# Kernel tuning notes

Measured on AMD Instinct MI355X. Metric: run time of the kernel, lower is better.

The kernel has to match this reference:

```python
import jax, jax.numpy as jnp
import numpy as np

DEPTH = 8
DIM = 1024
DI = 2 * DIM        # d_inner (expand=2)
DSTATE = 16         # d_state
DCONV = 4           # conv kernel width
DTRANK = DIM // 16  # dt_rank = ceil(d_model/16) = 64
B = 2
L = 2048
EPS = 1e-5


def setup_inputs() -> dict:
    key = jax.random.key(0)
    ks = jax.random.split(key, 8)
    s = 0.02
    A_log = jnp.broadcast_to(
        jnp.log(jnp.arange(1, DSTATE + 1, dtype=jnp.float32)), (DEPTH, DI, DSTATE)
    )
    return {
        "x": jax.random.normal(ks[0], (B, L, DIM), jnp.float32),
        "in_proj_w": jax.random.normal(ks[1], (DEPTH, 2 * DI, DIM), jnp.float32) * s,
        "conv_w": jax.random.normal(ks[2], (DEPTH, DI, DCONV), jnp.float32) * s,
        "conv_b": jnp.zeros((DEPTH, DI), jnp.float32),
        "x_proj_w": jax.random.normal(ks[3], (DEPTH, DTRANK + 2 * DSTATE, DI), jnp.float32) * s,
        "dt_proj_w": jax.random.normal(ks[4], (DEPTH, DI, DTRANK), jnp.float32) * s,
        "dt_proj_b": jax.random.normal(ks[5], (DEPTH, DI), jnp.float32) * 0.1,
        "A_log": A_log + 0.0,
        "D": jnp.ones((DEPTH, DI), jnp.float32),
        "out_proj_w": jax.random.normal(ks[6], (DEPTH, DIM, DI), jnp.float32) * s,
        "rms_w": jnp.ones((DEPTH, DIM), jnp.float32),
    }


def _selective_scan(xs, delta, Bm, Cm, A):
    # xs, delta: [B, L, DI]; Bm, Cm: [B, L, DSTATE]; A: [DI, DSTATE]
    def step(h, t):
        dt, Bt, Ct, xt = t  # [B,DI], [B,N], [B,N], [B,DI]
        dA = jnp.exp(dt[:, :, None] * A)                      # [B,DI,N]
        h = dA * h + (dt * xt)[:, :, None] * Bt[:, None, :]   # [B,DI,N]
        y = jnp.einsum('bdn,bn->bd', h, Ct)                   # [B,DI]
        return h, y

    h0 = jnp.zeros((xs.shape[0], xs.shape[2], A.shape[1]), xs.dtype)
    ts = (delta.transpose(1, 0, 2), Bm.transpose(1, 0, 2),
          Cm.transpose(1, 0, 2), xs.transpose(1, 0, 2))
    _, ys = jax.lax.scan(step, h0, ts)  # ys: [L,B,DI]
    return ys.transpose(1, 0, 2)


def _mamba(x, Wi, cw, cb, Wx, Wdt, bdt, A_log, Dp, Wo):
    # in_proj (no bias): [B,L,DIM] -> [B,L,2*DI]
    xz = jnp.einsum('bld,ed->ble', x, Wi)
    xs, z = jnp.split(xz, 2, axis=-1)
    # depthwise causal conv1d, kernel DCONV, left pad DCONV-1
    xc = jax.lax.conv_general_dilated(
        xs.transpose(0, 2, 1), cw[:, None, :], (1,), [(DCONV - 1, 0)],
        dimension_numbers=('NCH', 'OIH', 'NCH'), feature_group_count=DI)
    xs = jax.nn.silu(xc + cb[None, :, None]).transpose(0, 2, 1)  # [B,L,DI]
    # x_proj -> dt, B, C
    xdbl = jnp.einsum('bld,ed->ble', xs, Wx)
    dt, Bm, Cm = jnp.split(xdbl, [DTRANK, DTRANK + DSTATE], axis=-1)
    delta = jax.nn.softplus(jnp.einsum('blr,dr->bld', dt, Wdt) + bdt)  # [B,L,DI]
    A = -jnp.exp(A_log)  # [DI, DSTATE]
    y = _selective_scan(xs, delta, Bm, Cm, A) + xs * Dp
    y = y * jax.nn.silu(z)
    return jnp.einsum('bld,ed->ble', y, Wo)  # out_proj, no bias


def _rmsnorm(x, w):
    return x * jax.lax.rsqrt(jnp.mean(x * x, axis=-1, keepdims=True) + EPS) * w


def reference(x, in_proj_w, conv_w, conv_b, x_proj_w, dt_proj_w, dt_proj_b,
              A_log, D, out_proj_w, rms_w):
    for i in range(DEPTH):
        x = _mamba(x, in_proj_w[i], conv_w[i], conv_b[i], x_proj_w[i],
                   dt_proj_w[i], dt_proj_b[i], A_log[i], D[i], out_proj_w[i])
        x = _rmsnorm(x, rms_w[i])
    return x
```

## Files before the change

kernel.cpp:

```cpp
#include <hip/hip_runtime.h>
#include <cstddef>

#define DEPTH  8
#define DIMM   1024
#define DI     2048
#define NST    16
#define DCONVK 4
#define DTRANK 64
#define BB     2
#define LL     2048
#define MM     (BB*LL)
#define BD     (BB*DI)
#define CHK    32
#define LC     (LL/CHK)
#define LOG2E  1.44269504088896f

typedef __attribute__((ext_vector_type(8))) short bf16x8;
typedef __attribute__((ext_vector_type(4))) float f32x4;

__device__ __forceinline__ unsigned short f2bf(float f) {
  unsigned int u = __float_as_uint(f);
  unsigned int r = (u + 0x7fffu + ((u >> 16) & 1u)) >> 16;
  return (unsigned short)r;
}
__device__ __forceinline__ float bf2f(unsigned short h) {
  return __uint_as_float(((unsigned int)h) << 16);
}

__global__ __launch_bounds__(256) void cvt2_k(const float* __restrict__ x,
                                              unsigned short* __restrict__ p,
                                              size_t n) {
  size_t i = ((size_t)blockIdx.x * 256 + threadIdx.x) * 4;
  float4 v = *(const float4*)(x + i);
  float vv[4] = {v.x, v.y, v.z, v.w};
  unsigned short u1[4], u2[4];
#pragma unroll
  for (int k = 0; k < 4; ++k) {
    unsigned short h1 = f2bf(vv[k]);
    u1[k] = h1;
    u2[k] = f2bf(vv[k] - bf2f(h1));
  }
  *(ushort4*)(p + i)     = make_ushort4(u1[0], u1[1], u1[2], u1[3]);
  *(ushort4*)(p + n + i) = make_ushort4(u2[0], u2[1], u2[2], u2[3]);
}

template <int BN, int NSPLIT>
__global__ __launch_bounds__(512, 2) void gemm3ph(
    const unsigned short* __restrict__ Ap, int lda_a, int pstr_a,
    const unsigned short* __restrict__ Bp, int lda_b, int pstr_b,
    float* __restrict__ C0, float* __restrict__ C1, int N, int Ktot) {
  constexpr int BM  = 256;
  constexpr int BF  = BN / 64;
  constexpr int BL  = BN / 128;
  constexpr int RA1 = BM * 32;
  constexpr int RB0 = 2 * BM * 32;
  constexpr int RB1 = RB0 + BN * 32;
  constexpr int BUFS = (2 * BM + 2 * BN) * 32;
  __shared__ unsigned short S[2 * BUFS];

  const int t  = threadIdx.x;
  const int w  = t >> 6;
  const int l  = t & 63;
  const int lm = l & 15;
  const int qs = ((l >> 4) << 3) ^ (((lm >> 1) & 3) << 3);

  const int nx   = gridDim.x;
  const int nwg  = nx * gridDim.y;
  const int flat = blockIdx.y * nx + blockIdx.x;
  const int swz  = (flat & 7) * (nwg >> 3) + (flat >> 3);
  const int m0 = (swz / nx) * BM;
  const int n0 = (swz % nx) * BN;
  const int z  = (NSPLIT == 2) ? blockIdx.z : 0;
  const int KS = Ktot / NSPLIT;

  const int wm = (w & 1) << 7;
  const int wn = (w >> 1) * (BN / 4);

  const int rr = t >> 2;
  const int kq = ((t & 3) ^ ((rr >> 1) & 3)) << 3;
  const unsigned short* srcA = Ap + (size_t)(m0 + rr) * lda_a + (size_t)z * KS + kq;
  const unsigned short* srcB = Bp + (size_t)(n0 + rr) * lda_b + (size_t)z * KS + kq;
  const size_t a128 = (size_t)128 * lda_a;
  const size_t b128 = (size_t)128 * lda_b;
  const int dbase = (w << 6) * 8;

#define GI(p_, off_)                                                           \
  __builtin_amdgcn_global_load_lds(                                            \
      (const __attribute__((address_space(1))) unsigned int*)(p_),             \
      (__attribute__((address_space(3))) unsigned int*)&S[bnext + (off_) + dbase], \
      16, 0, 0)

#define GI_PH0(kb_)                                                            \
  { GI(srcA + (kb_), 0); GI(srcA + a128 + (kb_), 4096);                        \
    GI(srcB + (kb_), RB0);                                                     \
    if constexpr (BL == 2) GI(srcB + b128 + (kb_), RB0 + 4096); }

#define GI_PH1(kb_)                                                            \
  { GI(srcB + (size_t)pstr_b + (kb_), RB1);                                    \
    if constexpr (BL == 2) GI(srcB + (size_t)pstr_b + b128 + (kb_), RB1 + 4096); }

#define GI_PH2(kb_)                                                            \
  { GI(srcA + (size_t)pstr_a + (kb_), RA1);                                    \
    GI(srcA + (size_t)pstr_a + a128 + (kb_), RA1 + 4096); }

  f32x4 acc[8][BF];
#pragma unroll
  for (int i = 0; i < 8; ++i)
#pragma unroll
    for (int j = 0; j < BF; ++j) acc[i][j] = (f32x4){0.f, 0.f, 0.f, 0.f};

  {
    const int bnext = 0;
    GI_PH0((size_t)0);
    GI_PH1((size_t)0);
    GI_PH2((size_t)0);
  }
  if constexpr (BN == 256) asm volatile("s_waitcnt vmcnt(4)" ::: "memory");
  else                     asm volatile("s_waitcnt vmcnt(3)" ::: "memory");
  __builtin_amdgcn_s_barrier();

  const int NT = KS >> 5;
#pragma unroll 2
  for (int ti = 0; ti < NT; ++ti) {
    const int bcur  = (ti & 1) ? BUFS : 0;
    const int bnext = (ti & 1) ? 0 : BUFS;
    const size_t kb = (size_t)((ti + 1 < NT) ? (ti + 1) : 0) * 32;
    const unsigned short* Sb = &S[bcur];
    bf16x8 a[8], b0[BF], b1[BF];

#pragma unroll
    for (int i = 0; i < 8; ++i)
      a[i] = *(const bf16x8*)&Sb[(wm + i * 16 + lm) * 32 + qs];
#pragma unroll
    for (int j = 0; j < BF; ++j)
      b0[j] = *(const bf16x8*)&Sb[RB0 + (wn + j * 16 + lm) * 32 + qs];
    GI_PH0(kb);
    if constexpr (BN == 256) asm volatile("s_waitcnt vmcnt(6)" ::: "memory");
    else                     asm volatile("s_waitcnt vmcnt(5)" ::: "memory");
    __builtin_amdgcn_s_barrier();
    asm volatile("s_waitcnt lgkmcnt(0)" ::: "memory");
    __builtin_amdgcn_s_setprio(1);
#pragma unroll
    for (int i = 0; i < 8; ++i)
#pragma unroll
      for (int j = 0; j < BF; ++j)
        acc[i][j] = __builtin_amdgcn_mfma_f32_16x16x32_bf16(a[i], b0[j], acc[i][j], 0, 0, 0);
    __builtin_amdgcn_s_setprio(0);
    __builtin_amdgcn_s_barrier();

#pragma unroll
    for (int j = 0; j < BF; ++j)
      b1[j] = *(const bf16x8*)&Sb[RB1 + (wn + j * 16 + lm) * 32 + qs];
    GI_PH1(kb);
    if constexpr (BN == 256) asm volatile("s_waitcnt vmcnt(6)" ::: "memory");
    else                     asm volatile("s_waitcnt vmcnt(4)" ::: "memory");
    __builtin_amdgcn_s_barrier();
    asm volatile("s_waitcnt lgkmcnt(0)" ::: "memory");
    __builtin_amdgcn_s_setprio(1);
#pragma unroll
    for (int i = 0; i < 8; ++i)
#pragma unroll
      for (int j = 0; j < BF; ++j)
        acc[i][j] = __builtin_amdgcn_mfma_f32_16x16x32_bf16(a[i], b1[j], acc[i][j], 0, 0, 0);
    __builtin_amdgcn_s_setprio(0);
    __builtin_amdgcn_s_barrier();

#pragma unroll
    for (int i = 0; i < 8; ++i)
      a[i] = *(const bf16x8*)&Sb[RA1 + (wm + i * 16 + lm) * 32 + qs];
    GI_PH2(kb);
    if constexpr (BN == 256) asm volatile("s_waitcnt vmcnt(4)" ::: "memory");
    else                     asm volatile("s_waitcnt vmcnt(3)" ::: "memory");
    __builtin_amdgcn_s_barrier();
    asm volatile("s_waitcnt lgkmcnt(0)" ::: "memory");
    __builtin_amdgcn_s_setprio(1);
#pragma unroll
    for (int i = 0; i < 8; ++i)
#pragma unroll
      for (int j = 0; j < BF; ++j)
        acc[i][j] = __builtin_amdgcn_mfma_f32_16x16x32_bf16(a[i], b0[j], acc[i][j], 0, 0, 0);
    __builtin_amdgcn_s_setprio(0);
    __builtin_amdgcn_s_barrier();
  }
#undef GI_PH2
#undef GI_PH1
#undef GI_PH0
#undef GI

  float* Cc = (NSPLIT == 2 && blockIdx.z) ? C1 : C0;
  const int row0 = (l >> 4) << 2;
#pragma unroll
  for (int i = 0; i < 8; ++i)
#pragma unroll
    for (int j = 0; j < BF; ++j)
#pragma unroll
      for (int r = 0; r < 4; ++r) {
        int m = m0 + wm + i * 16 + row0 + r;
        int n = n0 + wn + j * 16 + lm;
        Cc[(size_t)m * N + n] = acc[i][j][r];
      }
}

__global__ __launch_bounds__(256) void dtproj_mp(const unsigned short* __restrict__ Ap,
                                                 const unsigned short* __restrict__ Bp,
                                                 const float* __restrict__ bdt,
                                                 float* __restrict__ Cd) {
  __shared__ unsigned short S[32768];
  const int t  = threadIdx.x;
  const int w  = t >> 6;
  const int l  = t & 63;
  const int lm = l & 15;
  const int q8 = (l >> 4) << 3;
  const int qs = q8 ^ (((lm >> 1) & 3) << 3);
  const int m0 = blockIdx.y * 128;
  const int n0 = blockIdx.x * 128;
  const int wm = (w & 1) << 6;
  const int wn = (w >> 1) << 6;

#pragma unroll
  for (int it = 0; it < 16; ++it) {
    int c  = it * 256 + t;
    int kt = c >> 11;
    int c2 = c & 2047;
    const unsigned short* base;
    int r, aslot;
    if (c2 < 1024) {
      int p = c2 >> 9; int wi = c2 & 511; r = wi >> 2; aslot = wi & 3;
      base = Ap + (size_t)p * (MM * 64) + (size_t)(m0 + r) * 64;
    } else {
      int c3 = c2 - 1024;
      int p = c3 >> 9; int wi = c3 & 511; r = wi >> 2; aslot = wi & 3;
      base = Bp + (size_t)p * (DI * 64) + (size_t)(n0 + r) * 64;
    }
    int kq = (aslot ^ ((r >> 1) & 3)) << 3;
    __builtin_amdgcn_global_load_lds(
        (const __attribute__((address_space(1))) unsigned int*)(base + kt * 32 + kq),
        (__attribute__((address_space(3))) unsigned int*)&S[(size_t)(it * 256 + (w << 6)) * 8],
        16, 0, 0);
  }
  __syncthreads();

  f32x4 acc[4][4];
#pragma unroll
  for (int i = 0; i < 4; ++i)
#pragma unroll
    for (int j = 0; j < 4; ++j) acc[i][j] = (f32x4){0.f, 0.f, 0.f, 0.f};

#pragma unroll
  for (int kt = 0; kt < 2; ++kt) {
    const int RA = kt * 16384;
    const int RB = kt * 16384 + 8192;
    bf16x8 a0[4], aX[4], b0[4];
#pragma unroll
    for (int i = 0; i < 4; ++i)
      a0[i] = *(const bf16x8*)&S[RA + (wm + i * 16 + lm) * 32 + qs];
#pragma unroll
    for (int j = 0; j < 4; ++j)
      b0[j] = *(const bf16x8*)&S[RB + (wn + j * 16 + lm) * 32 + qs];
#pragma unroll
    for (int i = 0; i < 4; ++i)
#pragma unroll
      for (int j = 0; j < 4; ++j)
        acc[i][j] = __builtin_amdgcn_mfma_f32_16x16x32_bf16(a0[i], b0[j], acc[i][j], 0, 0, 0);
#pragma unroll
    for (int j = 0; j < 4; ++j)
      aX[j] = *(const bf16x8*)&S[RB + 4096 + (wn + j * 16 + lm) * 32 + qs];
#pragma unroll
    for (int i = 0; i < 4; ++i)
#pragma unroll
      for (int j = 0; j < 4; ++j)
        acc[i][j] = __builtin_amdgcn_mfma_f32_16x16x32_bf16(a0[i], aX[j], acc[i][j], 0, 0, 0);
#pragma unroll
    for (int i = 0; i < 4; ++i)
      aX[i] = *(const bf16x8*)&S[RA + 4096 + (wm + i * 16 + lm) * 32 + qs];
#pragma unroll
    for (int i = 0; i < 4; ++i)
#pragma unroll
      for (int j = 0; j < 4; ++j)
        acc[i][j] = __builtin_amdgcn_mfma_f32_16x16x32_bf16(aX[i], b0[j], acc[i][j], 0, 0, 0);
  }

  const int row0 = (l >> 4) << 2;
#pragma unroll
  for (int j = 0; j < 4; ++j) {
    int n = n0 + wn + j * 16 + lm;
    float bv = bdt[n];
#pragma unroll
    for (int i = 0; i < 4; ++i)
#pragma unroll
      for (int r = 0; r < 4; ++r) {
        int m = m0 + wm + i * 16 + row0 + r;
        float x = acc[i][j][r] + bv;
        Cd[(size_t)m * DI + n] = fmaxf(x, 0.f) + log1pf(expf(-fabsf(x)));
      }
  }
}

#define XPN 96
__global__ __launch_bounds__(256) void xproj_part_k(const float* __restrict__ A,
                                                    const float* __restrict__ W,
                                                    float* __restrict__ Cp) {
  __shared__ float As[16][128];
  __shared__ float Ws[16][XPN];
  const int t  = threadIdx.x;
  const int tx = t & 15;
  const int ty = t >> 4;
  const int m0 = blockIdx.x * 128;
  const int kb = blockIdx.y * 256;
  float acc[8][6];
#pragma unroll
  for (int i = 0; i < 8; ++i)
#pragma unroll
    for (int j = 0; j < 6; ++j) acc[i][j] = 0.f;

  for (int k0 = kb; k0 < kb + 256; k0 += 16) {
#pragma unroll
    for (int e = t; e < 512; e += 256) {
      int r = e >> 2, cq = (e & 3) << 2;
      float4 v = *(const float4*)(A + (size_t)(m0 + r) * DI + k0 + cq);
      As[cq+0][r] = v.x; As[cq+1][r] = v.y; As[cq+2][r] = v.z; As[cq+3][r] = v.w;
    }
    for (int e = t; e < 384; e += 256) {
      int r = e >> 2, cq = (e & 3) << 2;
      float4 v = *(const float4*)(W + (size_t)r * DI + k0 + cq);
      Ws[cq+0][r] = v.x; Ws[cq+1][r] = v.y; Ws[cq+2][r] = v.z; Ws[cq+3][r] = v.w;
    }
    __syncthreads();
#pragma unroll
    for (int kk = 0; kk < 16; ++kk) {
      float a[8], b[6];
#pragma unroll
      for (int i = 0; i < 8; ++i) a[i] = As[kk][ty*8 + i];
#pragma unroll
      for (int j = 0; j < 6; ++j) b[j] = Ws[kk][tx*6 + j];
#pragma unroll
      for (int i = 0; i < 8; ++i)
#pragma unroll
        for (int j = 0; j < 6; ++j) acc[i][j] += a[i] * b[j];
    }
    __syncthreads();
  }
  float* cp = Cp + (size_t)blockIdx.y * MM * XPN;
#pragma unroll
  for (int i = 0; i < 8; ++i)
#pragma unroll
    for (int j = 0; j < 6; ++j)
      cp[(size_t)(m0 + ty*8 + i) * XPN + tx*6 + j] = acc[i][j];
}

__global__ __launch_bounds__(256) void xproj_red_k(const float* __restrict__ Cp,
                                                   float* __restrict__ o,
                                                   unsigned short* __restrict__ dtp) {
  int i = blockIdx.x * 256 + threadIdx.x;
  float s = 0.f;
#pragma unroll
  for (int ks = 0; ks < 8; ++ks) s += Cp[(size_t)ks * (MM * XPN) + i];
  o[i] = s;
  int m = i / 96, col = i - m * 96;
  if (col < DTRANK) {
    unsigned short h1 = f2bf(s);
    dtp[(size_t)m * DTRANK + col] = h1;
    dtp[(size_t)MM * DTRANK + (size_t)m * DTRANK + col] = f2bf(s - bf2f(h1));
  }
}

__device__ __forceinline__ float fast_silu(float x) {
  return x * __builtin_amdgcn_rcpf(1.f + exp2f(-LOG2E * x));
}

__global__ __launch_bounds__(256) void conv_silu_k(const float* __restrict__ xz,
                                                   const float* __restrict__ cw,
                                                   const float* __restrict__ cb,
                                                   float* __restrict__ xc) {
  int idx = blockIdx.x * 256 + threadIdx.x;
  int c  = idx & (DI - 1);
  int bl = idx >> 11;
  int l  = bl & (LL - 1);
  float acc = cb[c];
#pragma unroll
  for (int k = 0; k < DCONVK; ++k) {
    int ls = l - (DCONVK - 1) + k;
    if (ls >= 0)
      acc += xz[(size_t)(bl - (DCONVK - 1) + k) * (2*DI) + c] * cw[c*DCONVK + k];
  }
  xc[idx] = fast_silu(acc);
}

__global__ __launch_bounds__(256) void scan_pass1(const float* __restrict__ delta,
                                                  const float* __restrict__ xc,
                                                  const float* __restrict__ xdbl,
                                                  const float* __restrict__ A_log,
                                                  float* __restrict__ Hc,
                                                  float* __restrict__ Sdt) {
  const int t  = threadIdx.x;
  const int c  = blockIdx.x >> 6;
  const int g  = blockIdx.x & 63;
  const int q  = t >> 2;
  const int nq = t & 3;
  const int ch = g * 64 + q;
  const int b  = ch >> 11;
  const int d  = ch & (DI - 1);
  const size_t rowbase = (size_t)b * LL + (size_t)c * LC;

  __shared__ float Bs[LC * 16];
  { int row = t >> 2, seg = t & 3;
    *(float4*)&Bs[row * 16 + seg * 4] =
        *(const float4*)(xdbl + (rowbase + row) * 96 + DTRANK + seg * 4);
  }
  __syncthreads();

  float4 al = *(const float4*)(A_log + (size_t)d * NST + nq * 4);
  const float Av0 = -expf(al.x) * LOG2E, Av1 = -expf(al.y) * LOG2E;
  const float Av2_ = -expf(al.z) * LOG2E, Av3 = -expf(al.w) * LOG2E;
  float h0 = 0.f, h1 = 0.f, h2 = 0.f, h3 = 0.f, S = 0.f;

#define P1_SU 4
  float aD[P1_SU], aX[P1_SU];
  float bD[P1_SU], bX[P1_SU];

#define P1_LOAD(l0, D_, X_)                                            \
  { _Pragma("unroll")                                                  \
    for (int u = 0; u < P1_SU; ++u) {                                  \
      size_t bl = rowbase + (l0) + u;                                  \
      D_[u] = delta[bl * DI + d];                                      \
      X_[u] = xc[bl * DI + d];                                         \
    } }

#define P1_COMP(l0, D_, X_)                                            \
  { _Pragma("unroll")                                                  \
    for (int u = 0; u < P1_SU; ++u) {                                  \
      float4 Bv = *(const float4*)&Bs[((l0) + u) * 16 + nq * 4];       \
      float dt = D_[u], uB = dt * X_[u];                               \
      h0 = fmaf(exp2f(dt * Av0), h0, uB * Bv.x);                       \
      h1 = fmaf(exp2f(dt * Av1), h1, uB * Bv.y);                       \
      h2 = fmaf(exp2f(dt * Av2_), h2, uB * Bv.z);                      \
      h3 = fmaf(exp2f(dt * Av3), h3, uB * Bv.w);                       \
      S += dt;                                                         \
    } }

  P1_LOAD(0, aD, aX);
  for (int l0 = 0; l0 < LC; l0 += 2 * P1_SU) {
    P1_LOAD(l0 + P1_SU, bD, bX);
    P1_COMP(l0, aD, aX);
    if (l0 + 2 * P1_SU < LC) P1_LOAD(l0 + 2 * P1_SU, aD, aX);
    P1_COMP(l0 + P1_SU, bD, bX);
  }
#undef P1_LOAD
#undef P1_COMP
  size_t hi = ((size_t)c * BD + ch) * NST + nq * 4;
  float4 hv; hv.x = h0; hv.y = h1; hv.z = h2; hv.w = h3;
  *(float4*)(Hc + hi) = hv;
  if (nq == 0) Sdt[(size_t)c * BD + ch] = S;
}

__global__ __launch_bounds__(256) void scan_pass2(float* __restrict__ Hc,
                                                  const float* __restrict__ Sdt,
                                                  const float* __restrict__ A_log) {
  const int g  = blockIdx.x * 256 + threadIdx.x;
  const int n  = g & (NST - 1);
  const int ch = g >> 4;
  const int d  = ch & (DI - 1);
  const float Av2 = -expf(A_log[d * NST + n]) * LOG2E;
  float Sv[CHK];
#pragma unroll
  for (int c = 0; c < CHK; ++c) Sv[c] = Sdt[(size_t)c * BD + ch];
  float h = 0.f;
  float tmp = Hc[(size_t)ch * NST + n];
#pragma unroll
  for (int c = 0; c < CHK; ++c) {
    size_t idx = ((size_t)c * BD + ch) * NST + n;
    float tnext = (c + 1 < CHK) ? Hc[((size_t)(c+1) * BD + ch) * NST + n] : 0.f;
    Hc[idx] = h;
    h = fmaf(exp2f(Av2 * Sv[c]), h, tmp);
    tmp = tnext;
  }
}

__global__ __launch_bounds__(256) void scan_pass3(const float* __restrict__ delta,
                                                  const float* __restrict__ xc,
                                                  const float* __restrict__ xdbl,
                                                  const float* __restrict__ A_log,
                                                  float* __restrict__ xzp,
                                                  const float* __restrict__ Dp,
                                                  const float* __restrict__ Hc) {
  const int t  = threadIdx.x;
  const int c  = blockIdx.x >> 6;
  const int g  = blockIdx.x & 63;
  const int q  = t >> 2;
  const int nq = t & 3;
  const int ch = g * 64 + q;
  const int b  = ch >> 11;
  const int d  = ch & (DI - 1);
  const int dbs = (g & 31) * 64;
  const size_t rowbase = (size_t)b * LL + (size_t)c * LC;

  __shared__ float BCs[LC * 32];
  __shared__ unsigned short Y1s[LC][64];
  __shared__ unsigned short Y2s[LC][64];
  {
#pragma unroll
    for (int e = t; e < 512; e += 256) {
      int row = e >> 3, seg = e & 7;
      *(float4*)&BCs[row * 32 + seg * 4] =
          *(const float4*)(xdbl + (rowbase + row) * 96 + DTRANK + seg * 4);
    }
  }
  __syncthreads();

  float4 al = *(const float4*)(A_log + (size_t)d * NST + nq * 4);
  const float Av0 = -expf(al.x) * LOG2E, Av1 = -expf(al.y) * LOG2E;
  const float Av2_ = -expf(al.z) * LOG2E, Av3 = -expf(al.w) * LOG2E;
  const float Dv = Dp[d];
  float4 hv = *(const float4*)(Hc + ((size_t)c * BD + ch) * NST + nq * 4);
  float h0 = hv.x, h1 = hv.y, h2 = hv.z, h3 = hv.w;

#define P3_SU 2
  float aD[P3_SU], aX[P3_SU], aZ[P3_SU];
  float bD[P3_SU], bX[P3_SU], bZ[P3_SU];

#define P3_LOAD(l0, D_, X_, Z_)                                        \
  { _Pragma("unroll")                                                  \
    for (int u = 0; u < P3_SU; ++u) {                                  \
      size_t bl = rowbase + (l0) + u;                                  \
      D_[u] = delta[bl * DI + d];                                      \
      X_[u] = xc[bl * DI + d];                                         \
      Z_[u] = xzp[bl * (2*DI) + DI + d];                               \
    } }

#define P3_COMP(l0, D_, X_, Z_)                                        \
  { _Pragma("unroll")                                                  \
    for (int u = 0; u < P3_SU; ++u) {                                  \
      float4 Bv = *(const float4*)&BCs[((l0) + u) * 32 + nq * 4];      \
      float4 Cv = *(const float4*)&BCs[((l0) + u) * 32 + 16 + nq * 4]; \
      float dt = D_[u], uB = dt * X_[u];                               \
      h0 = fmaf(exp2f(dt * Av0), h0, uB * Bv.x);                       \
      h1 = fmaf(exp2f(dt * Av1), h1, uB * Bv.y);                       \
      h2 = fmaf(exp2f(dt * Av2_), h2, uB * Bv.z);                      \
      h3 = fmaf(exp2f(dt * Av3), h3, uB * Bv.w);                       \
      float s = fmaf(h1, Cv.y, h0 * Cv.x);                             \
      float t2 = fmaf(h3, Cv.w, h2 * Cv.z);                            \
      s += t2;                                                         \
      s += __shfl_xor(s, 1, 4);                                        \
      s += __shfl_xor(s, 2, 4);                                        \
      if (nq == 0) {                                                   \
        float yv = (s + X_[u] * Dv) * fast_silu(Z_[u]);                \
        unsigned short y1 = f2bf(yv);                                  \
        Y1s[(l0) + u][q] = y1;                                         \
        Y2s[(l0) + u][q] = f2bf(yv - bf2f(y1));                        \
      }                                                                \
    } }

  P3_LOAD(0, aD, aX, aZ);
  for (int l0 = 0; l0 < LC; l0 += 2 * P3_SU) {
    P3_LOAD(l0 + P3_SU, bD, bX, bZ);
    P3_COMP(l0, aD, aX, aZ);
    if (l0 + 2 * P3_SU < LC) P3_LOAD(l0 + 2 * P3_SU, aD, aX, aZ);
    P3_COMP(l0 + P3_SU, bD, bX, bZ);
  }
#undef P3_LOAD
#undef P3_COMP
  __syncthreads();

  unsigned short* yp = (unsigned short*)xzp;
#pragma unroll
  for (int e = t; e < LC * 16; e += 256) {
    int row = e >> 4, seg = (e & 15) << 2;
    size_t base = (rowbase + row) * 8192 + dbs + seg;
    *(ushort4*)(yp + base)        = *(const ushort4*)&Y1s[row][seg];
    *(ushort4*)(yp + base + 2048) = *(const ushort4*)&Y2s[row][seg];
  }
}

template <bool PLANES>
__global__ __launch_bounds__(256) void rmsnorm_k(const float* __restrict__ x,
                                                 const float* __restrict__ x2,
                                                 const float* __restrict__ w,
                                                 float* __restrict__ o,
                                                 unsigned short* __restrict__ op) {
  int row = blockIdx.x;
  const float* xr  = x  + (size_t)row * DIMM;
  const float* x2r = x2 + (size_t)row * DIMM;
  float s = 0.f;
  for (int i = threadIdx.x; i < DIMM; i += 256) {
    float v = xr[i] + x2r[i]; s += v * v;
  }
#pragma unroll
  for (int off = 32; off > 0; off >>= 1) s += __shfl_xor(s, off, 64);
  __shared__ float red[4];
  if ((threadIdx.x & 63) == 0) red[threadIdx.x >> 6] = s;
  __syncthreads();
  float tot = red[0] + red[1] + red[2] + red[3];
  float scale = rsqrtf(tot * (1.0f / DIMM) + 1e-5f);
  for (int i = threadIdx.x; i < DIMM; i += 256) {
    float v = (xr[i] + x2r[i]) * scale * w[i];
    if (PLANES) {
      unsigned short h1 = f2bf(v);
      op[(size_t)row * DIMM + i] = h1;
      op[(size_t)MM * DIMM + (size_t)row * DIMM + i] = f2bf(v - bf2f(h1));
    } else {
      o[(size_t)row * DIMM + i] = v;
    }
  }
}

extern "C" void kernel_launch(void* const* d_in, const int* in_sizes, int n_in,
                              void* d_out, int out_size, void* d_ws, size_t ws_size,
                              hipStream_t stream) {
  (void)in_sizes; (void)n_in; (void)out_size; (void)ws_size;
  const float* x_in    = (const float*)d_in[0];
  const float* Wi_all  = (const float*)d_in[1];
  const float* cw_all  = (const float*)d_in[2];
  const float* cb_all  = (const float*)d_in[3];
  const float* Wx_all  = (const float*)d_in[4];
  const float* Wdt_all = (const float*)d_in[5];
  const float* bdt_all = (const float*)d_in[6];
  const float* Alog_all= (const float*)d_in[7];
  const float* D_all   = (const float*)d_in[8];
  const float* Wo_all  = (const float*)d_in[9];
  const float* rw_all  = (const float*)d_in[10];
  float* out = (float*)d_out;

  float* ws    = (float*)d_ws;
  float* xz    = ws;
  float* xc    = xz   + (size_t)MM * 2 * DI;
  float* xdbl  = xc   + (size_t)MM * DI;
  float* delta = xdbl + (size_t)MM * 96;
  float* xbuf  = delta+ (size_t)MM * DI;
  float* outtmp = xc;

  unsigned short* xpl  = (unsigned short*)delta;
  unsigned short* wipl = (unsigned short*)xc;
  unsigned short* wopl = (unsigned short*)(xc + (size_t)4194304);
  float*          Cp   = delta;
  float* part1 = delta + (size_t)4194304;
  float* Hc   = xbuf;
  float* Sdt  = Hc + (size_t)CHK * BD * NST;
  unsigned short* dtpl  = (unsigned short*)(xbuf + 2228224);
  unsigned short* wdtpl = (unsigned short*)(xbuf + 2490368);

  const int EW_GRID = (MM * DI) / 256;
  const int SCAN_GRID = CHK * 64;

  for (int i = 0; i < DEPTH; ++i) {
    const float* Wi   = Wi_all  + (size_t)i * (2*DI) * DIMM;
    const float* cw   = cw_all  + (size_t)i * DI * DCONVK;
    const float* cb   = cb_all  + (size_t)i * DI;
    const float* Wx   = Wx_all  + (size_t)i * 96 * DI;
    const float* Wdt  = Wdt_all + (size_t)i * DI * DTRANK;
    const float* bdt  = bdt_all + (size_t)i * DI;
    const float* Alog = Alog_all+ (size_t)i * DI * NST;
    const float* Dp   = D_all   + (size_t)i * DI;
    const float* Wo   = Wo_all  + (size_t)i * DIMM * DI;
    const float* rw   = rw_all  + (size_t)i * DIMM;

    if (i == 0)
      cvt2_k<<<(MM*DIMM)/1024, 256, 0, stream>>>(x_in, xpl, (size_t)MM * DIMM);
    cvt2_k<<<((2*DI)*DIMM)/1024, 256, 0, stream>>>(Wi, wipl, (size_t)(2*DI) * DIMM);
    gemm3ph<256,1><<<dim3((2*DI)/256, MM/256, 1), 512, 0, stream>>>(
        xpl, DIMM, MM*DIMM, wipl, DIMM, (2*DI)*DIMM, xz, nullptr, 2*DI, DIMM);
    conv_silu_k<<<EW_GRID, 256, 0, stream>>>(xz, cw, cb, xc);
    xproj_part_k<<<dim3(MM/128, 8), 256, 0, stream>>>(xc, Wx, Cp);
    xproj_red_k<<<(MM*XPN)/256, 256, 0, stream>>>(Cp, xdbl, dtpl);
    cvt2_k<<<(DI*DTRANK)/1024, 256, 0, stream>>>(Wdt, wdtpl, (size_t)DI * DTRANK);
    dtproj_mp<<<dim3(DI/128, MM/128), 256, 0, stream>>>(dtpl, wdtpl, bdt, delta);
    scan_pass1<<<SCAN_GRID, 256, 0, stream>>>(delta, xc, xdbl, Alog, Hc, Sdt);
    scan_pass2<<<(BD*NST)/256, 256, 0, stream>>>(Hc, Sdt, Alog);
    scan_pass3<<<SCAN_GRID, 256, 0, stream>>>(delta, xc, xdbl, Alog, xz, Dp, Hc);
    cvt2_k<<<(DIMM*DI)/1024, 256, 0, stream>>>(Wo, wopl, (size_t)DIMM * DI);
    gemm3ph<128,2><<<dim3(DIMM/128, MM/256, 2), 512, 0, stream>>>(
        (const unsigned short*)xz, 8192, 2048, wopl, DI, DIMM*DI,
        outtmp, part1, DIMM, DI);
    if (i < DEPTH - 1)
      rmsnorm_k<true><<<MM, 256, 0, stream>>>(outtmp, part1, rw, nullptr, xpl);
    else
      rmsnorm_k<false><<<MM, 256, 0, stream>>>(outtmp, part1, rw, out, nullptr);
  }
}
```

Before: 3.222 ms.

## Map one channel per thread in chunked scan, holding all 16 states

```diff
diff --git a/kernel.cpp b/kernel.cpp
--- a/kernel.cpp
+++ b/kernel.cpp
@@ -393,11 +393,9 @@
                                                   float* __restrict__ Hc,
                                                   float* __restrict__ Sdt) {
   const int t  = threadIdx.x;
-  const int c  = blockIdx.x >> 6;
-  const int g  = blockIdx.x & 63;
-  const int q  = t >> 2;
-  const int nq = t & 3;
-  const int ch = g * 64 + q;
+  const int g  = blockIdx.x;
+  const int c  = blockIdx.y;
+  const int ch = g * 256 + t;
   const int b  = ch >> 11;
   const int d  = ch & (DI - 1);
   const size_t rowbase = (size_t)b * LL + (size_t)c * LC;
@@ -409,10 +407,19 @@
   }
   __syncthreads();
 
-  float4 al = *(const float4*)(A_log + (size_t)d * NST + nq * 4);
-  const float Av0 = -expf(al.x) * LOG2E, Av1 = -expf(al.y) * LOG2E;
-  const float Av2_ = -expf(al.z) * LOG2E, Av3 = -expf(al.w) * LOG2E;
-  float h0 = 0.f, h1 = 0.f, h2 = 0.f, h3 = 0.f, S = 0.f;
+  float Av[NST];
+#pragma unroll
+  for (int n4 = 0; n4 < 4; ++n4) {
+    float4 al = *(const float4*)(A_log + (size_t)d * NST + n4 * 4);
+    Av[n4*4+0] = -expf(al.x) * LOG2E;
+    Av[n4*4+1] = -expf(al.y) * LOG2E;
+    Av[n4*4+2] = -expf(al.z) * LOG2E;
+    Av[n4*4+3] = -expf(al.w) * LOG2E;
+  }
+  float h[NST];
+#pragma unroll
+  for (int n = 0; n < NST; ++n) h[n] = 0.f;
+  float S = 0.f;
 
 #define P1_SU 4
   float aD[P1_SU], aX[P1_SU];
@@ -429,12 +436,16 @@
 #define P1_COMP(l0, D_, X_)                                            \
   { _Pragma("unroll")                                                  \
     for (int u = 0; u < P1_SU; ++u) {                                  \
-      float4 Bv = *(const float4*)&Bs[((l0) + u) * 16 + nq * 4];       \
       float dt = D_[u], uB = dt * X_[u];                               \
-      h0 = fmaf(exp2f(dt * Av0), h0, uB * Bv.x);                       \
-      h1 = fmaf(exp2f(dt * Av1), h1, uB * Bv.y);                       \
-      h2 = fmaf(exp2f(dt * Av2_), h2, uB * Bv.z);                      \
-      h3 = fmaf(exp2f(dt * Av3), h3, uB * Bv.w);                       \
+      const f32x4* B4 = (const f32x4*)&Bs[((l0) + u) * 16];            \
+      f32x4 B0 = B4[0], B1 = B4[1], B2 = B4[2], B3 = B4[3];            \
+      _Pragma("unroll")                                                \
+      for (int n = 0; n < 4; ++n) {                                    \
+        h[n]      = fmaf(exp2f(dt * Av[n]),      h[n],      uB * B0[n]); \
+        h[4 + n]  = fmaf(exp2f(dt * Av[4 + n]),  h[4 + n],  uB * B1[n]); \
+        h[8 + n]  = fmaf(exp2f(dt * Av[8 + n]),  h[8 + n],  uB * B2[n]); \
+        h[12 + n] = fmaf(exp2f(dt * Av[12 + n]), h[12 + n], uB * B3[n]); \
+      }                                                                \
       S += dt;                                                         \
     } }
 
@@ -447,10 +458,13 @@
   }
 #undef P1_LOAD
 #undef P1_COMP
-  size_t hi = ((size_t)c * BD + ch) * NST + nq * 4;
-  float4 hv; hv.x = h0; hv.y = h1; hv.z = h2; hv.w = h3;
-  *(float4*)(Hc + hi) = hv;
-  if (nq == 0) Sdt[(size_t)c * BD + ch] = S;
+
+  float* hp = Hc + ((size_t)c * BD + ch) * NST;
+#pragma unroll
+  for (int n4 = 0; n4 < 4; ++n4)
+    *(float4*)(hp + n4 * 4) =
+        make_float4(h[n4*4], h[n4*4+1], h[n4*4+2], h[n4*4+3]);
+  Sdt[(size_t)c * BD + ch] = S;
 }
 
 __global__ __launch_bounds__(256) void scan_pass2(float* __restrict__ Hc,
@@ -484,19 +498,14 @@
                                                   const float* __restrict__ Dp,
                                                   const float* __restrict__ Hc) {
   const int t  = threadIdx.x;
-  const int c  = blockIdx.x >> 6;
-  const int g  = blockIdx.x & 63;
-  const int q  = t >> 2;
-  const int nq = t & 3;
-  const int ch = g * 64 + q;
+  const int g  = blockIdx.x;
+  const int c  = blockIdx.y;
+  const int ch = g * 256 + t;
   const int b  = ch >> 11;
   const int d  = ch & (DI - 1);
-  const int dbs = (g & 31) * 64;
   const size_t rowbase = (size_t)b * LL + (size_t)c * LC;
 
   __shared__ float BCs[LC * 32];
-  __shared__ unsigned short Y1s[LC][64];
-  __shared__ unsigned short Y2s[LC][64];
   {
 #pragma unroll
     for (int e = t; e < 512; e += 256) {
@@ -507,12 +516,25 @@
   }
   __syncthreads();
 
-  float4 al = *(const float4*)(A_log + (size_t)d * NST + nq * 4);
-  const float Av0 = -expf(al.x) * LOG2E, Av1 = -expf(al.y) * LOG2E;
-  const float Av2_ = -expf(al.z) * LOG2E, Av3 = -expf(al.w) * LOG2E;
+  float Av[NST];
+#pragma unroll
+  for (int n4 = 0; n4 < 4; ++n4) {
+    float4 al = *(const float4*)(A_log + (size_t)d * NST + n4 * 4);
+    Av[n4*4+0] = -expf(al.x) * LOG2E;
+    Av[n4*4+1] = -expf(al.y) * LOG2E;
+    Av[n4*4+2] = -expf(al.z) * LOG2E;
+    Av[n4*4+3] = -expf(al.w) * LOG2E;
+  }
   const float Dv = Dp[d];
-  float4 hv = *(const float4*)(Hc + ((size_t)c * BD + ch) * NST + nq * 4);
-  float h0 = hv.x, h1 = hv.y, h2 = hv.z, h3 = hv.w;
+  float h[NST];
+  { const float* hp = Hc + ((size_t)c * BD + ch) * NST;
+#pragma unroll
+    for (int n4 = 0; n4 < 4; ++n4) {
+      float4 hv = *(const float4*)(hp + n4 * 4);
+      h[n4*4+0] = hv.x; h[n4*4+1] = hv.y; h[n4*4+2] = hv.z; h[n4*4+3] = hv.w;
+    }
+  }
+  unsigned short* yp = (unsigned short*)xzp;
 
 #define P3_SU 2
   float aD[P3_SU], aX[P3_SU], aZ[P3_SU];
@@ -530,24 +552,32 @@
 #define P3_COMP(l0, D_, X_, Z_)                                        \
   { _Pragma("unroll")                                                  \
     for (int u = 0; u < P3_SU; ++u) {                                  \
-      float4 Bv = *(const float4*)&BCs[((l0) + u) * 32 + nq * 4];      \
-      float4 Cv = *(const float4*)&BCs[((l0) + u) * 32 + 16 + nq * 4]; \
       float dt = D_[u], uB = dt * X_[u];                               \
-      h0 = fmaf(exp2f(dt * Av0), h0, uB * Bv.x);                       \
-      h1 = fmaf(exp2f(dt * Av1), h1, uB * Bv.y);                       \
-      h2 = fmaf(exp2f(dt * Av2_), h2, uB * Bv.z);                      \
-      h3 = fmaf(exp2f(dt * Av3), h3, uB * Bv.w);                       \
-      float s = fmaf(h1, Cv.y, h0 * Cv.x);                             \
-      float t2 = fmaf(h3, Cv.w, h2 * Cv.z);                            \
-      s += t2;                                                         \
-      s += __shfl_xor(s, 1, 4);                                        \
-      s += __shfl_xor(s, 2, 4);                                        \
-      if (nq == 0) {                                                   \
-        float yv = (s + X_[u] * Dv) * fast_silu(Z_[u]);                \
-        unsigned short y1 = f2bf(yv);                                  \
-        Y1s[(l0) + u][q] = y1;                                         \
-        Y2s[(l0) + u][q] = f2bf(yv - bf2f(y1));                        \
+      const f32x4* R4 = (const f32x4*)&BCs[((l0) + u) * 32];           \
+      f32x4 B0 = R4[0], B1 = R4[1], B2 = R4[2], B3 = R4[3];            \
+      f32x4 C0 = R4[4], C1 = R4[5], C2 = R4[6], C3 = R4[7];            \
+      _Pragma("unroll")                                                \
+      for (int n = 0; n < 4; ++n) {                                    \
+        h[n]      = fmaf(exp2f(dt * Av[n]),      h[n],      uB * B0[n]); \
+        h[4 + n]  = fmaf(exp2f(dt * Av[4 + n]),  h[4 + n],  uB * B1[n]); \
+        h[8 + n]  = fmaf(exp2f(dt * Av[8 + n]),  h[8 + n],  uB * B2[n]); \
+        h[12 + n] = fmaf(exp2f(dt * Av[12 + n]), h[12 + n], uB * B3[n]); \
       }                                                                \
+        \
+      float p0 = fmaf(h[1],  C0[1], h[0]  * C0[0]);                    \
+      p0 += fmaf(h[3],  C0[3], h[2]  * C0[2]);                         \
+      float p1 = fmaf(h[5],  C1[1], h[4]  * C1[0]);                    \
+      p1 += fmaf(h[7],  C1[3], h[6]  * C1[2]);                         \
+      float p2 = fmaf(h[9],  C2[1], h[8]  * C2[0]);                    \
+      p2 += fmaf(h[11], C2[3], h[10] * C2[2]);                         \
+      float p3 = fmaf(h[13], C3[1], h[12] * C3[0]);                    \
+      p3 += fmaf(h[15], C3[3], h[14] * C3[2]);                         \
+      float s = (p0 + p1) + (p2 + p3);                                 \
+      float yv = (s + X_[u] * Dv) * fast_silu(Z_[u]);                  \
+      unsigned short y1 = f2bf(yv);                                    \
+      size_t yb = (rowbase + (l0) + u) * 8192 + d;                     \
+      yp[yb] = y1;                                                     \
+      yp[yb + 2048] = f2bf(yv - bf2f(y1));                             \
     } }
 
   P3_LOAD(0, aD, aX, aZ);
@@ -559,16 +589,6 @@
   }
 #undef P3_LOAD
 #undef P3_COMP
-  __syncthreads();
-
-  unsigned short* yp = (unsigned short*)xzp;
-#pragma unroll
-  for (int e = t; e < LC * 16; e += 256) {
-    int row = e >> 4, seg = (e & 15) << 2;
-    size_t base = (rowbase + row) * 8192 + dbs + seg;
-    *(ushort4*)(yp + base)        = *(const ushort4*)&Y1s[row][seg];
-    *(ushort4*)(yp + base + 2048) = *(const ushort4*)&Y2s[row][seg];
-  }
 }
 
 template <bool PLANES>
@@ -639,7 +659,6 @@
   unsigned short* wdtpl = (unsigned short*)(xbuf + 2490368);
 
   const int EW_GRID = (MM * DI) / 256;
-  const int SCAN_GRID = CHK * 64;
 
   for (int i = 0; i < DEPTH; ++i) {
     const float* Wi   = Wi_all  + (size_t)i * (2*DI) * DIMM;
@@ -663,9 +682,9 @@
     xproj_red_k<<<(MM*XPN)/256, 256, 0, stream>>>(Cp, xdbl, dtpl);
     cvt2_k<<<(DI*DTRANK)/1024, 256, 0, stream>>>(Wdt, wdtpl, (size_t)DI * DTRANK);
     dtproj_mp<<<dim3(DI/128, MM/128), 256, 0, stream>>>(dtpl, wdtpl, bdt, delta);
-    scan_pass1<<<SCAN_GRID, 256, 0, stream>>>(delta, xc, xdbl, Alog, Hc, Sdt);
+    scan_pass1<<<dim3(BD/256, CHK), 256, 0, stream>>>(delta, xc, xdbl, Alog, Hc, Sdt);
     scan_pass2<<<(BD*NST)/256, 256, 0, stream>>>(Hc, Sdt, Alog);
-    scan_pass3<<<SCAN_GRID, 256, 0, stream>>>(delta, xc, xdbl, Alog, xz, Dp, Hc);
+    scan_pass3<<<dim3(BD/256, CHK), 256, 0, stream>>>(delta, xc, xdbl, Alog, xz, Dp, Hc);
     cvt2_k<<<(DIMM*DI)/1024, 256, 0, stream>>>(Wo, wopl, (size_t)DIMM * DI);
     gemm3ph<128,2><<<dim3(DIMM/128, MM/256, 2), 512, 0, stream>>>(
         (const unsigned short*)xz, 8192, 2048, wopl, DI, DIMM*DI,
```

Result: no change. 3.238 ms (+0.5%).
